# Kernel tuning notes

Hardware: AMD Instinct MI355X
Metric: run time of the kernel (lower is better)

Reference implementation:

```python
import jax, jax.numpy as jnp
import numpy as np

GRID_SIDES = (16, 32, 64)  # levels=3, base_grid_size=16, expansion=2.0, grid_dimensions=2
BATCH, INPUT_DIM = 8192, 256


def setup_inputs() -> dict:
    key = jax.random.key(0)
    k0, k1, k2, k3 = jax.random.split(key, 4)
    x = jax.random.normal(k0, (BATCH, INPUT_DIM), dtype=jnp.float32)
    w1 = jax.random.normal(k1, (GRID_SIDES[0] ** 2, INPUT_DIM), dtype=jnp.float32)
    w2 = jax.random.normal(k2, (GRID_SIDES[1] ** 2, INPUT_DIM), dtype=jnp.float32)
    w3 = jax.random.normal(k3, (GRID_SIDES[2] ** 2, INPUT_DIM), dtype=jnp.float32)
    return {"x": x, "w1": w1, "w2": w2, "w3": w3}


def _som_level(x, w, side):
    # Squared Euclidean distances (B, N) via the expanded form; N = side*side.
    d2 = (
        jnp.sum(x * x, axis=1, keepdims=True)
        - 2.0 * (x @ w.T)
        + jnp.sum(w * w, axis=1)
    )
    bmu_flat = jnp.argmin(d2, axis=1)  # (B,)
    coords = jnp.stack(jnp.unravel_index(bmu_flat, (side, side)), axis=-1)  # (B, 2)
    # Quantization error = exact Euclidean distance to the BMU prototype.
    diff = x - w[bmu_flat]  # (B, D)
    q_err = jnp.sqrt(jnp.sum(diff * diff, axis=1))  # (B,)
    return coords, q_err


def reference(x, w1, w2, w3):
    c1, q1 = _som_level(x, w1, GRID_SIDES[0])
    c2, q2 = _som_level(x, w2, GRID_SIDES[1])
    c3, q3 = _som_level(x, w3, GRID_SIDES[2])
    return (c1, c2, c3, q1, q2, q3)
```

## Files before the change

### kernel.cpp

```cpp
#include <hip/hip_runtime.h>
#include <hip/hip_fp16.h>
#include <stdint.h>

#define DIM 256
#define KE  768
#define NW  5376

typedef _Float16 half8 __attribute__((ext_vector_type(8)));
typedef float floatx4 __attribute__((ext_vector_type(4)));

#define WS_WE_OFF    12582912
#define WS_WNORM_OFF 20840448
#define WS_XNORM_OFF 20861952
#define WS_BEST_OFF  20894720

__global__ __launch_bounds__(256) void conv_kernel(
    const float* __restrict__ x, const float* __restrict__ w1,
    const float* __restrict__ w2, const float* __restrict__ w3,
    ushort* __restrict__ Xe, ushort* __restrict__ We,
    float* __restrict__ wnorm, float* __restrict__ xnorm) {
  int task = blockIdx.x * 4 + (threadIdx.x >> 6);
  int lane = threadIdx.x & 63;
  const float* src; ushort* dst; float* ndst; int isx;
  if (task < 8192) {
    src = x + (size_t)task * DIM; dst = Xe + (size_t)task * KE;
    ndst = xnorm + task; isx = 1;
  } else {
    int wi = task - 8192;
    if (wi < 256)       src = w1 + (size_t)wi * DIM;
    else if (wi < 1280) src = w2 + (size_t)(wi - 256) * DIM;
    else                src = w3 + (size_t)(wi - 1280) * DIM;
    dst = We + (size_t)wi * KE; ndst = wnorm + wi; isx = 0;
  }
  float4 v = *(const float4*)(src + lane * 4);
  float fv[4] = {v.x, v.y, v.z, v.w};
  float s = fv[0]*fv[0] + fv[1]*fv[1] + fv[2]*fv[2] + fv[3]*fv[3];
  #pragma unroll
  for (int o = 32; o > 0; o >>= 1) s += __shfl_xor(s, o);
  if (lane == 0) *ndst = s;

  ushort h[4], l[4];
  #pragma unroll
  for (int e = 0; e < 4; ++e) {
    __half hh = __float2half(fv[e]);
    float hf = __half2float(hh);
    __half ll = __float2half((fv[e] - hf) * 2048.0f);
    h[e] = __half_as_ushort(hh);
    l[e] = __half_as_ushort(ll);
  }
  ushort4 h4 = make_ushort4(h[0], h[1], h[2], h[3]);
  ushort4 l4 = make_ushort4(l[0], l[1], l[2], l[3]);
  if (isx) {
    *(ushort4*)(dst + lane * 4)        = h4;
    *(ushort4*)(dst + 256 + lane * 4)  = h4;
    *(ushort4*)(dst + 512 + lane * 4)  = l4;
  } else {
    *(ushort4*)(dst + lane * 4)        = h4;
    *(ushort4*)(dst + 256 + lane * 4)  = l4;
    *(ushort4*)(dst + 512 + lane * 4)  = h4;
  }
}

__global__ __launch_bounds__(256) void gemm_kernel(
    const ushort* __restrict__ Xe, const ushort* __restrict__ We,
    const float* __restrict__ xnorm, const float* __restrict__ wnorm,
    unsigned long long* __restrict__ best) {
  __shared__ __align__(16) ushort As[128 * 64];
  __shared__ __align__(16) ushort Bs[128 * 64];
  __shared__ unsigned long long red[2][128];

  const int cb = blockIdx.x;
  const int r0 = blockIdx.y * 128;
  const int n0 = cb * 128;
  int level, lbase;
  if (cb < 2)       { level = 0; lbase = 0; }
  else if (cb < 10) { level = 1; lbase = 256; }
  else              { level = 2; lbase = 1280; }

  const int t = threadIdx.x;
  const int w = t >> 6;
  const int lane = t & 63;
  const int ln = lane & 15, q = lane >> 4;
  const int wm = (w >> 1) * 64, wn = (w & 1) * 64;

  floatx4 acc[4][4];
  #pragma unroll
  for (int i = 0; i < 4; ++i)
    #pragma unroll
    for (int j = 0; j < 4; ++j) acc[i][j] = (floatx4)0.0f;

  for (int k0 = 0; k0 < KE; k0 += 64) {
    if (k0 == 256) {
      #pragma unroll
      for (int i = 0; i < 4; ++i)
        #pragma unroll
        for (int j = 0; j < 4; ++j) acc[i][j] *= 2048.0f;
    }
    #pragma unroll
    for (int it = 0; it < 4; ++it) {
      int p = it * 256 + t;
      int m = p >> 3;
      int c = (p & 7) ^ (m & 7);
      const ushort* ga = Xe + (size_t)(r0 + m) * KE + k0 + c * 8;
      const ushort* gb = We + (size_t)(n0 + m) * KE + k0 + c * 8;
      int lbase_chunks = it * 256 + (t & 192);
      __builtin_amdgcn_global_load_lds(
          (const __attribute__((address_space(1))) void*)ga,
          (__attribute__((address_space(3))) void*)(As + lbase_chunks * 8), 16, 0, 0);
      __builtin_amdgcn_global_load_lds(
          (const __attribute__((address_space(1))) void*)gb,
          (__attribute__((address_space(3))) void*)(Bs + lbase_chunks * 8), 16, 0, 0);
    }
    __syncthreads();
    #pragma unroll
    for (int s = 0; s < 2; ++s) {
      half8 a[4], b[4];
      #pragma unroll
      for (int mt = 0; mt < 4; ++mt) {
        int m = wm + mt * 16 + ln;
        int pos = m * 8 + ((s * 4 + q) ^ (m & 7));
        a[mt] = *(const half8*)&As[pos * 8];
      }
      #pragma unroll
      for (int nt = 0; nt < 4; ++nt) {
        int n = wn + nt * 16 + ln;
        int pos = n * 8 + ((s * 4 + q) ^ (n & 7));
        b[nt] = *(const half8*)&Bs[pos * 8];
      }
      #pragma unroll
      for (int mt = 0; mt < 4; ++mt)
        #pragma unroll
        for (int nt = 0; nt < 4; ++nt)
          acc[mt][nt] = __builtin_amdgcn_mfma_f32_16x16x32_f16(
              a[mt], b[nt], acc[mt][nt], 0, 0, 0);
    }
    __syncthreads();
  }

  float wnv[4];
  #pragma unroll
  for (int nt = 0; nt < 4; ++nt) wnv[nt] = wnorm[n0 + wn + nt * 16 + ln];

  #pragma unroll
  for (int mt = 0; mt < 4; ++mt) {
    #pragma unroll
    for (int r = 0; r < 4; ++r) {
      int rowl = wm + mt * 16 + q * 4 + r;
      float xnv = xnorm[r0 + rowl];
      unsigned long long bp = ~0ull;
      #pragma unroll
      for (int nt = 0; nt < 4; ++nt) {
        float d2 = fmaxf(xnv + wnv[nt] - acc[mt][nt][r] * 0.0009765625f, 0.0f);
        unsigned col = (unsigned)(n0 + wn + nt * 16 + ln - lbase);
        unsigned long long p =
            ((unsigned long long)__float_as_uint(d2) << 32) | col;
        bp = (p < bp) ? p : bp;
      }
      #pragma unroll
      for (int off = 1; off < 16; off <<= 1) {
        unsigned long long o = __shfl_xor(bp, off);
        bp = (o < bp) ? o : bp;
      }
      if (ln == 0) red[w & 1][rowl] = bp;
    }
  }
  __syncthreads();
  if (t < 128) {
    unsigned long long a = red[0][t], b = red[1][t];
    unsigned long long m = (a < b) ? a : b;
    atomicMin(&best[level * 8192 + r0 + t], m);
  }
}

__global__ __launch_bounds__(256) void finalize_kernel(
    const float* __restrict__ x, const float* __restrict__ w1,
    const float* __restrict__ w2, const float* __restrict__ w3,
    const unsigned long long* __restrict__ best, float* __restrict__ out) {
  int task = blockIdx.x * 4 + (threadIdx.x >> 6);
  int lane = threadIdx.x & 63;
  int level = task >> 13;
  int row = task & 8191;
  const float* w; unsigned side;
  if (level == 0)      { w = w1; side = 16; }
  else if (level == 1) { w = w2; side = 32; }
  else                 { w = w3; side = 64; }
  unsigned idx = (unsigned)(best[level * 8192 + row] & 0xFFFFFFFFull);
  float4 xv = *(const float4*)(x + (size_t)row * DIM + lane * 4);
  float4 wv = *(const float4*)(w + (size_t)idx * DIM + lane * 4);
  float dx = xv.x - wv.x, dy = xv.y - wv.y, dz = xv.z - wv.z, dw = xv.w - wv.w;
  float s = dx * dx + dy * dy + dz * dz + dw * dw;
  #pragma unroll
  for (int o = 32; o > 0; o >>= 1) s += __shfl_xor(s, o);
  if (lane == 0) {
    out[level * 16384 + row * 2 + 0] = (float)(idx / side);
    out[level * 16384 + row * 2 + 1] = (float)(idx % side);
    out[49152 + level * 8192 + row] = sqrtf(s);
  }
}

extern "C" void kernel_launch(void* const* d_in, const int* in_sizes, int n_in,
                              void* d_out, int out_size, void* d_ws, size_t ws_size,
                              hipStream_t stream) {
  const float* x  = (const float*)d_in[0];
  const float* w1 = (const float*)d_in[1];
  const float* w2 = (const float*)d_in[2];
  const float* w3 = (const float*)d_in[3];
  ushort* Xe = (ushort*)d_ws;
  ushort* We = (ushort*)((char*)d_ws + WS_WE_OFF);
  float* wnorm = (float*)((char*)d_ws + WS_WNORM_OFF);
  float* xnorm = (float*)((char*)d_ws + WS_XNORM_OFF);
  unsigned long long* best = (unsigned long long*)((char*)d_ws + WS_BEST_OFF);

  hipMemsetAsync(best, 0xFF, 24576 * sizeof(unsigned long long), stream);
  conv_kernel<<<3392, 256, 0, stream>>>(x, w1, w2, w3, Xe, We, wnorm, xnorm);
  gemm_kernel<<<dim3(42, 64), 256, 0, stream>>>(Xe, We, xnorm, wnorm, best);
  finalize_kernel<<<6144, 256, 0, stream>>>(x, w1, w2, w3, best, (float*)d_out);
}
```

Baseline: 164.4 us.

## Reuse GEMM distance in finalize, fold best init into conv kernel

The finalize kernel now takes the quantization error from the squared distance already packed in the GEMM's argmin result, instead of re-gathering x and the BMU prototype and recomputing the exact distance. The memset of the best buffer moves into the conversion kernel, removing one launch. The GEMM reduction scratch now aliases the A tile in shared memory, and the k-loop is peeled around the rescale step. The risk is that the error now comes from the expanded-form, split-fp16 distance rather than an exact difference, so it may lose precision.

Measured after the change: 180.5 us. +9.8%, slower.

```diff
diff --git a/kernel.cpp b/kernel.cpp
--- a/kernel.cpp
+++ b/kernel.cpp
@@ -4,7 +4,6 @@
 
 #define DIM 256
 #define KE  768
-#define NW  5376
 
 typedef _Float16 half8 __attribute__((ext_vector_type(8)));
 typedef float floatx4 __attribute__((ext_vector_type(4)));
@@ -18,7 +17,10 @@
     const float* __restrict__ x, const float* __restrict__ w1,
     const float* __restrict__ w2, const float* __restrict__ w3,
     ushort* __restrict__ Xe, ushort* __restrict__ We,
-    float* __restrict__ wnorm, float* __restrict__ xnorm) {
+    float* __restrict__ wnorm, float* __restrict__ xnorm,
+    unsigned long long* __restrict__ best) {
+  if (blockIdx.x < 96) best[blockIdx.x * 256 + threadIdx.x] = ~0ull;
+
   int task = blockIdx.x * 4 + (threadIdx.x >> 6);
   int lane = threadIdx.x & 63;
   const float* src; ushort* dst; float* ndst; int isx;
@@ -67,7 +69,6 @@
     unsigned long long* __restrict__ best) {
   __shared__ __align__(16) ushort As[128 * 64];
   __shared__ __align__(16) ushort Bs[128 * 64];
-  __shared__ unsigned long long red[2][128];
 
   const int cb = blockIdx.x;
   const int r0 = blockIdx.y * 128;
@@ -89,13 +90,7 @@
     #pragma unroll
     for (int j = 0; j < 4; ++j) acc[i][j] = (floatx4)0.0f;
 
-  for (int k0 = 0; k0 < KE; k0 += 64) {
-    if (k0 == 256) {
-      #pragma unroll
-      for (int i = 0; i < 4; ++i)
-        #pragma unroll
-        for (int j = 0; j < 4; ++j) acc[i][j] *= 2048.0f;
-    }
+  auto kchunk = [&](int k0) {
     #pragma unroll
     for (int it = 0; it < 4; ++it) {
       int p = it * 256 + t;
@@ -135,11 +130,20 @@
               a[mt], b[nt], acc[mt][nt], 0, 0, 0);
     }
     __syncthreads();
-  }
+  };
+
+  for (int k0 = 0; k0 < 256; k0 += 64) kchunk(k0);
+  #pragma unroll
+  for (int i = 0; i < 4; ++i)
+    #pragma unroll
+    for (int j = 0; j < 4; ++j) acc[i][j] *= 2048.0f;
+  for (int k0 = 256; k0 < KE; k0 += 64) kchunk(k0);
 
   float wnv[4];
   #pragma unroll
   for (int nt = 0; nt < 4; ++nt) wnv[nt] = wnorm[n0 + wn + nt * 16 + ln];
+
+  unsigned long long* red = (unsigned long long*)As;
 
   #pragma unroll
   for (int mt = 0; mt < 4; ++mt) {
@@ -161,41 +165,29 @@
         unsigned long long o = __shfl_xor(bp, off);
         bp = (o < bp) ? o : bp;
       }
-      if (ln == 0) red[w & 1][rowl] = bp;
+      if (ln == 0) red[(w & 1) * 128 + rowl] = bp;
     }
   }
   __syncthreads();
   if (t < 128) {
-    unsigned long long a = red[0][t], b = red[1][t];
+    unsigned long long a = red[t], b = red[128 + t];
     unsigned long long m = (a < b) ? a : b;
     atomicMin(&best[level * 8192 + r0 + t], m);
   }
 }
 
 __global__ __launch_bounds__(256) void finalize_kernel(
-    const float* __restrict__ x, const float* __restrict__ w1,
-    const float* __restrict__ w2, const float* __restrict__ w3,
     const unsigned long long* __restrict__ best, float* __restrict__ out) {
-  int task = blockIdx.x * 4 + (threadIdx.x >> 6);
-  int lane = threadIdx.x & 63;
+  int task = blockIdx.x * 256 + threadIdx.x;
   int level = task >> 13;
   int row = task & 8191;
-  const float* w; unsigned side;
-  if (level == 0)      { w = w1; side = 16; }
-  else if (level == 1) { w = w2; side = 32; }
-  else                 { w = w3; side = 64; }
-  unsigned idx = (unsigned)(best[level * 8192 + row] & 0xFFFFFFFFull);
-  float4 xv = *(const float4*)(x + (size_t)row * DIM + lane * 4);
-  float4 wv = *(const float4*)(w + (size_t)idx * DIM + lane * 4);
-  float dx = xv.x - wv.x, dy = xv.y - wv.y, dz = xv.z - wv.z, dw = xv.w - wv.w;
-  float s = dx * dx + dy * dy + dz * dz + dw * dw;
-  #pragma unroll
-  for (int o = 32; o > 0; o >>= 1) s += __shfl_xor(s, o);
-  if (lane == 0) {
-    out[level * 16384 + row * 2 + 0] = (float)(idx / side);
-    out[level * 16384 + row * 2 + 1] = (float)(idx % side);
-    out[49152 + level * 8192 + row] = sqrtf(s);
-  }
+  unsigned side = (level == 0) ? 16u : (level == 1) ? 32u : 64u;
+  unsigned long long p = best[task];
+  unsigned idx = (unsigned)(p & 0xFFFFFFFFull);
+  float d2 = __uint_as_float((unsigned)(p >> 32));
+  out[level * 16384 + row * 2 + 0] = (float)(idx / side);
+  out[level * 16384 + row * 2 + 1] = (float)(idx % side);
+  out[49152 + level * 8192 + row] = sqrtf(d2);
 }
 
 extern "C" void kernel_launch(void* const* d_in, const int* in_sizes, int n_in,
@@ -211,8 +203,7 @@
   float* xnorm = (float*)((char*)d_ws + WS_XNORM_OFF);
   unsigned long long* best = (unsigned long long*)((char*)d_ws + WS_BEST_OFF);
 
-  hipMemsetAsync(best, 0xFF, 24576 * sizeof(unsigned long long), stream);
-  conv_kernel<<<3392, 256, 0, stream>>>(x, w1, w2, w3, Xe, We, wnorm, xnorm);
+  conv_kernel<<<3392, 256, 0, stream>>>(x, w1, w2, w3, Xe, We, wnorm, xnorm, best);
   gemm_kernel<<<dim3(42, 64), 256, 0, stream>>>(Xe, We, xnorm, wnorm, best);
-  finalize_kernel<<<6144, 256, 0, stream>>>(x, w1, w2, w3, best, (float*)d_out);
-}
+  finalize_kernel<<<96, 256, 0, stream>>>(best, (float*)d_out);
+}
```
